# Optimization experiments

Hardware: AMD Instinct MI355X
Metric: run time of the kernel (lower is better)

## Reference

```python
import jax, jax.numpy as jnp
import numpy as np

RADIUS = 8
EPS = 1e-4


def box1d(x, r, axis):
    # sliding-window sum of width 2r+1 with border clamping (cumsum trick),
    # matching the classic guided-filter boxfilter (same as torch cumsum impl).
    n = x.shape[axis]
    c = jnp.cumsum(x, axis=axis)
    pad_shape = list(x.shape)
    pad_shape[axis] = 1
    s = jnp.concatenate([jnp.zeros(pad_shape, x.dtype), c], axis=axis)  # prefix sums, s[0]=0
    i = jnp.arange(n)
    hi = jnp.clip(i + r, 0, n - 1) + 1
    lo = jnp.clip(i - r - 1, -1, n - 1) + 1
    return jnp.take(s, hi, axis=axis) - jnp.take(s, lo, axis=axis)


def boxfilter2d(x, r):
    return box1d(box1d(x, r, -2), r, -1)


def setup_inputs() -> dict:
    key = jax.random.key(0)
    k1, k2 = jax.random.split(key)
    x = jax.random.uniform(k1, (4, 4, 1024, 1024), dtype=jnp.float32)
    guide = jax.random.uniform(k2, (4, 3, 1024, 1024), dtype=jnp.float32)
    return {"x": x, "guide": guide}


def guidedfilter2d_color(guide, src, r, eps):
    B, C, H, W = src.shape
    N = boxfilter2d(jnp.ones((B, 1, H, W), src.dtype), r)          # (B,1,H,W)
    mean_I = boxfilter2d(guide, r) / N                              # (B,3,H,W)
    mean_p = boxfilter2d(src, r) / N                                # (B,C,H,W)

    Ip = guide[:, :, None] * src[:, None]                           # (B,3,C,H,W)
    mean_Ip = boxfilter2d(Ip, r) / N[:, None]                       # (B,3,C,H,W)
    cov_Ip = mean_Ip - mean_I[:, :, None] * mean_p[:, None]         # (B,3,C,H,W)

    II = guide[:, :, None] * guide[:, None]                         # (B,3,3,H,W)
    var_I = boxfilter2d(II, r) / N[:, None] - mean_I[:, :, None] * mean_I[:, None]
    # eps added on the diagonal only, as in the torch code
    rr = var_I[:, 0, 0] + eps
    rg = var_I[:, 0, 1]
    rb = var_I[:, 0, 2]
    gg = var_I[:, 1, 1] + eps
    gb = var_I[:, 1, 2]
    bb = var_I[:, 2, 2] + eps

    det = (rr * gg * bb + 2.0 * rg * gb * rb
           - rb * gg * rb - rg * rg * bb - rr * gb * gb)            # (B,H,W)
    inv_rr = (gg * bb - gb * gb) / det
    inv_rg = -(rg * bb - rb * gb) / det
    inv_rb = (rg * gb - rb * gg) / det
    inv_gg = (rr * bb - rb * rb) / det
    inv_gb = -(rr * gb - rb * rg) / det
    inv_bb = (rr * gg - rg * rg) / det

    inv_sigma = jnp.stack([
        jnp.stack([inv_rr, inv_rg, inv_rb], 1),
        jnp.stack([inv_rg, inv_gg, inv_gb], 1),
        jnp.stack([inv_rb, inv_gb, inv_bb], 1),
    ], 1)                                                            # (B,3,3,H,W)

    a = jnp.einsum('bichw,bijhw->bjchw', cov_Ip, inv_sigma)          # (B,3,C,H,W)
    b = mean_p - jnp.einsum('bichw,bihw->bchw', a, mean_I)           # (B,C,H,W)

    mean_a = boxfilter2d(a, r) / N[:, None]                          # (B,3,C,H,W)
    mean_b = boxfilter2d(b, r) / N                                   # (B,C,H,W)

    q = jnp.einsum('bichw,bihw->bchw', mean_a, guide) + mean_b       # (B,C,H,W)
    return q


def reference(x, guide):
    return guidedfilter2d_color(guide, x, RADIUS, EPS)
```

## Files before the change

### kernel.cpp

```cpp
#include <hip/hip_runtime.h>

#define HH 1024
#define WW 1024
#define RAD 8
#define EPSF 1e-4f
#define HWSZ (HH * WW)
#define NPLB 16
#define T2 216
#define NTL 5
#define RROWS 4
#define V3R 32

__device__ __forceinline__ float4 f4add(float4 a, float4 b) {
  return make_float4(a.x + b.x, a.y + b.y, a.z + b.z, a.w + b.w);
}
__device__ __forceinline__ float4 f4sub(float4 a, float4 b) {
  return make_float4(a.x - b.x, a.y - b.y, a.z - b.z, a.w - b.w);
}
__device__ __forceinline__ float4 f4mul(float4 a, float4 b) {
  return make_float4(a.x * b.x, a.y * b.y, a.z * b.z, a.w * b.w);
}

__device__ __forceinline__ float wave_incl_scan(float v) {
  int t;
  t = __builtin_amdgcn_update_dpp(0, __float_as_int(v), 0x111, 0xf, 0xf, false);
  v += __int_as_float(t);
  t = __builtin_amdgcn_update_dpp(0, __float_as_int(v), 0x112, 0xf, 0xf, false);
  v += __int_as_float(t);
  t = __builtin_amdgcn_update_dpp(0, __float_as_int(v), 0x114, 0xf, 0xf, false);
  v += __int_as_float(t);
  t = __builtin_amdgcn_update_dpp(0, __float_as_int(v), 0x118, 0xf, 0xf, false);
  v += __int_as_float(t);
  t = __builtin_amdgcn_update_dpp(0, __float_as_int(v), 0x142, 0xa, 0xf, false);
  v += __int_as_float(t);
  t = __builtin_amdgcn_update_dpp(0, __float_as_int(v), 0x143, 0xc, 0xf, false);
  v += __int_as_float(t);
  return v;
}

__global__ __launch_bounds__(256, 2) void k_stats_solve(
    const float* __restrict__ x, const float* __restrict__ g,
    float* __restrict__ ws, int b0) {
  const int lane = threadIdx.x & 63;
  const int w = threadIdx.x >> 6;
  const int bi = blockIdx.y;
  const int gw = blockIdx.x * 4 + w;
  const int rowblk = gw / NTL;
  const int tix = gw - rowblk * NTL;
  const int y0 = rowblk * RROWS;
  const int b = b0 + bi;
  float* wsb = ws + (size_t)bi * NPLB * HWSZ;
  const int F = tix * T2;
  const int E = F - 20;
  const int relmax = (WW - 1) - E;
  const int col0 = E + 4 * lane;
  const bool ldok = (col0 >= 0) && (col0 < WW);

  const float* gp0 = g + (size_t)(b * 3 + 0) * HWSZ;
  const float* gp1 = g + (size_t)(b * 3 + 1) * HWSZ;
  const float* gp2 = g + (size_t)(b * 3 + 2) * HWSZ;
  const float* sp0 = x + (size_t)(b * 4 + 0) * HWSZ;
  const float* sp1 = x + (size_t)(b * 4 + 1) * HWSZ;
  const float* sp2 = x + (size_t)(b * 4 + 2) * HWSZ;
  const float* sp3 = x + (size_t)(b * 4 + 3) * HWSZ;

  const int cbase = E + 12 + 4 * lane;
  float nxinv[4];
#pragma unroll
  for (int j = 0; j < 4; ++j) {
    const int c = cbase + j;
    const int nx = min(c + RAD, WW - 1) - max(c - RAD, 0) + 1;
    nxinv[j] = 1.0f / (float)nx;
  }
  const bool abok = (lane <= 58) && (cbase >= 0) && (cbase < WW);
  const int qmax = relmax - 12;
  const int nstore = min(54, (WW - F) >> 2);
  const bool stok = lane < nstore;

  float4 s[25];
#pragma unroll
  for (int i = 0; i < 25; ++i) s[i] = make_float4(0.f, 0.f, 0.f, 0.f);

  const float4 Z4 = make_float4(0.f, 0.f, 0.f, 0.f);

  auto row_acc = [&](int yy, bool add) {
    if (yy < 0 || yy >= HH) return;
    const int off = yy * WW + col0;
    const float4 G0 = ldok ? *(const float4*)(gp0 + off) : Z4;
    const float4 G1 = ldok ? *(const float4*)(gp1 + off) : Z4;
    const float4 G2 = ldok ? *(const float4*)(gp2 + off) : Z4;
    const float4 S0 = ldok ? *(const float4*)(sp0 + off) : Z4;
    const float4 S1 = ldok ? *(const float4*)(sp1 + off) : Z4;
    const float4 S2 = ldok ? *(const float4*)(sp2 + off) : Z4;
    const float4 S3 = ldok ? *(const float4*)(sp3 + off) : Z4;
#define ACC(idx, val)                          \
  do {                                         \
    const float4 t_ = (val);                   \
    s[idx] = add ? f4add(s[idx], t_) : f4sub(s[idx], t_); \
  } while (0)
    ACC(0, G0); ACC(1, G1); ACC(2, G2);
    ACC(3, S0); ACC(4, S1); ACC(5, S2); ACC(6, S3);
    ACC(7, f4mul(G0, S0)); ACC(8, f4mul(G0, S1));
    ACC(9, f4mul(G0, S2)); ACC(10, f4mul(G0, S3));
    ACC(11, f4mul(G1, S0)); ACC(12, f4mul(G1, S1));
    ACC(13, f4mul(G1, S2)); ACC(14, f4mul(G1, S3));
    ACC(15, f4mul(G2, S0)); ACC(16, f4mul(G2, S1));
    ACC(17, f4mul(G2, S2)); ACC(18, f4mul(G2, S3));
    ACC(19, f4mul(G0, G0)); ACC(20, f4mul(G0, G1)); ACC(21, f4mul(G0, G2));
    ACC(22, f4mul(G1, G1)); ACC(23, f4mul(G1, G2)); ACC(24, f4mul(G2, G2));
#undef ACC
  };

  auto hbox4 = [&](float4 sv) -> float4 {
    const float s1 = sv.x + sv.y, s2 = s1 + sv.z, ts = s2 + sv.w;
    const float incl = wave_incl_scan(ts);
    const float base = incl - ts;
    const float P0 = base + sv.x, P1 = base + s1, P2 = base + s2, P3 = incl;
    const float PW = __shfl(P3, min(relmax >> 2, 63));
    const float h0 = __shfl(P0, lane + 5), h1 = __shfl(P1, lane + 5);
    const float h2 = __shfl(P2, lane + 5), h3 = __shfl(P3, lane + 5);
    const float l1 = __shfl(P0, lane + 1), l2 = __shfl(P1, lane + 1);
    const float l3 = __shfl(P2, lane + 1);
    const int r0 = 4 * lane + 12;
    float4 o;
    o.x = ((r0 + 8 <= relmax) ? h0 : PW) - ((E + r0 >= 9) ? P3 : 0.f);
    o.y = ((r0 + 9 <= relmax) ? h1 : PW) - ((E + r0 + 1 >= 9) ? l1 : 0.f);
    o.z = ((r0 + 10 <= relmax) ? h2 : PW) - ((E + r0 + 2 >= 9) ? l2 : 0.f);
    o.w = ((r0 + 11 <= relmax) ? h3 : PW) - ((E + r0 + 3 >= 9) ? l3 : 0.f);
    return o;
  };

  for (int yy = y0 - RAD; yy <= y0 + RAD; ++yy) row_acc(yy, true);

  for (int row = y0; row < y0 + RROWS; ++row) {
    const int ny = min(row + RAD, HH - 1) - max(row - RAD, 0) + 1;
    const float invny = 1.0f / (float)ny;
    float invN[4];
#pragma unroll
    for (int j = 0; j < 4; ++j) invN[j] = invny * nxinv[j];

    float mI[3][4];
#pragma unroll
    for (int k = 0; k < 3; ++k) {
      const float4 t = hbox4(s[k]);
      mI[k][0] = t.x * invN[0]; mI[k][1] = t.y * invN[1];
      mI[k][2] = t.z * invN[2]; mI[k][3] = t.w * invN[3];
    }
    float inv[6][4];
    {
      const float4 t19 = hbox4(s[19]), t20 = hbox4(s[20]), t21 = hbox4(s[21]);
      const float4 t22 = hbox4(s[22]), t23 = hbox4(s[23]), t24 = hbox4(s[24]);
      const float v19[4] = {t19.x, t19.y, t19.z, t19.w};
      const float v20[4] = {t20.x, t20.y, t20.z, t20.w};
      const float v21[4] = {t21.x, t21.y, t21.z, t21.w};
      const float v22[4] = {t22.x, t22.y, t22.z, t22.w};
      const float v23[4] = {t23.x, t23.y, t23.z, t23.w};
      const float v24[4] = {t24.x, t24.y, t24.z, t24.w};
#pragma unroll
      for (int j = 0; j < 4; ++j) {
        const float rr = v19[j] * invN[j] - mI[0][j] * mI[0][j] + EPSF;
        const float rg = v20[j] * invN[j] - mI[0][j] * mI[1][j];
        const float rb = v21[j] * invN[j] - mI[0][j] * mI[2][j];
        const float gg = v22[j] * invN[j] - mI[1][j] * mI[1][j] + EPSF;
        const float gb = v23[j] * invN[j] - mI[1][j] * mI[2][j];
        const float bb = v24[j] * invN[j] - mI[2][j] * mI[2][j] + EPSF;
        const float det = rr * gg * bb + 2.f * rg * gb * rb
                        - rb * gg * rb - rg * rg * bb - rr * gb * gb;
        const float idet = 1.0f / det;
        inv[0][j] = (gg * bb - gb * gb) * idet;
        inv[1][j] = (rb * gb - rg * bb) * idet;
        inv[2][j] = (rg * gb - rb * gg) * idet;
        inv[3][j] = (rr * bb - rb * rb) * idet;
        inv[4][j] = (rb * rg - rr * gb) * idet;
        inv[5][j] = (rr * gg - rg * rg) * idet;
      }
    }

    const size_t obase = (size_t)row * WW + F + 4 * lane;
    auto phaseB = [&](float4 vv, int plane) {
      const float s1 = vv.x + vv.y, s2 = s1 + vv.z, ts = s2 + vv.w;
      const float incl = wave_incl_scan(ts);
      const float base = incl - ts;
      const float Q0 = base + vv.x, Q1 = base + s1, Q2 = base + s2, Q3 = incl;
      const float PW2 = __shfl(Q3, min(qmax >> 2, 63));
      const float h0 = __shfl(Q0, lane + 4), h1 = __shfl(Q1, lane + 4);
      const float h2 = __shfl(Q2, lane + 4), h3 = __shfl(Q3, lane + 4);
      const float lm1 = __shfl(Q3, lane - 1);
      const int qf0 = 8 + 4 * lane;
      float4 o;
      o.x = ((qf0 + 8 <= qmax) ? h0 : PW2) - ((qf0 >= 9) ? lm1 : 0.f);
      o.y = ((qf0 + 9 <= qmax) ? h1 : PW2) - Q0;
      o.z = ((qf0 + 10 <= qmax) ? h2 : PW2) - Q1;
      o.w = ((qf0 + 11 <= qmax) ? h3 : PW2) - Q2;
      if (stok) *(float4*)(wsb + (size_t)plane * HWSZ + obase) = o;
    };

#pragma unroll
    for (int cc = 0; cc < 4; ++cc) {
      const float4 tmp = hbox4(s[3 + cc]);
      const float4 tq0 = hbox4(s[7 + cc]);
      const float4 tq1 = hbox4(s[11 + cc]);
      const float4 tq2 = hbox4(s[15 + cc]);
      const float mp[4] = {tmp.x, tmp.y, tmp.z, tmp.w};
      const float q0[4] = {tq0.x, tq0.y, tq0.z, tq0.w};
      const float q1[4] = {tq1.x, tq1.y, tq1.z, tq1.w};
      const float q2[4] = {tq2.x, tq2.y, tq2.z, tq2.w};
      float4 a0v, a1v, a2v, bv;
      float* pa0 = &a0v.x; float* pa1 = &a1v.x;
      float* pa2 = &a2v.x; float* pbv = &bv.x;
#pragma unroll
      for (int j = 0; j < 4; ++j) {
        const float m = mp[j] * invN[j];
        const float c0v = q0[j] * invN[j] - mI[0][j] * m;
        const float c1v = q1[j] * invN[j] - mI[1][j] * m;
        const float c2v = q2[j] * invN[j] - mI[2][j] * m;
        const float a0 = c0v * inv[0][j] + c1v * inv[1][j] + c2v * inv[2][j];
        const float a1 = c0v * inv[1][j] + c1v * inv[3][j] + c2v * inv[4][j];
        const float a2 = c0v * inv[2][j] + c1v * inv[4][j] + c2v * inv[5][j];
        const float b_ = m - (a0 * mI[0][j] + a1 * mI[1][j] + a2 * mI[2][j]);
        pa0[j] = abok ? a0 : 0.f;
        pa1[j] = abok ? a1 : 0.f;
        pa2[j] = abok ? a2 : 0.f;
        pbv[j] = abok ? b_ : 0.f;
      }
      phaseB(a0v, cc);
      phaseB(a1v, 4 + cc);
      phaseB(a2v, 8 + cc);
      phaseB(bv, 12 + cc);
    }

    row_acc(row + RAD + 1, true);
    row_acc(row - RAD, false);
  }
}

__global__ __launch_bounds__(256) void k_vbox_comb(const float* __restrict__ ws_,
                                                   const float* __restrict__ g,
                                                   float* __restrict__ out, int b0) {
  const int col = blockIdx.x * 256 + threadIdx.x;
  const int y0 = blockIdx.y * V3R;
  const int b = b0 + blockIdx.z;
  const float* wsb = ws_ + (size_t)blockIdx.z * NPLB * HWSZ;
  const float* gp0 = g + (size_t)(b * 3 + 0) * HWSZ;
  const float* gp1 = g + (size_t)(b * 3 + 1) * HWSZ;
  const float* gp2 = g + (size_t)(b * 3 + 2) * HWSZ;
  float* op0 = out + (size_t)(b * 4 + 0) * HWSZ;
  float* op1 = out + (size_t)(b * 4 + 1) * HWSZ;
  float* op2 = out + (size_t)(b * 4 + 2) * HWSZ;
  float* op3 = out + (size_t)(b * 4 + 3) * HWSZ;

  float acc[16];
#pragma unroll
  for (int i = 0; i < 16; ++i) acc[i] = 0.f;

  auto row_op = [&](int y, bool add) {
    const int off = y * WW + col;
#pragma unroll
    for (int i = 0; i < 16; ++i) {
      const float v = wsb[(size_t)i * HWSZ + off];
      acc[i] = add ? (acc[i] + v) : (acc[i] - v);
    }
  };

  for (int yy = y0 - RAD; yy <= y0 + RAD; ++yy)
    if (yy >= 0 && yy < HH) row_op(yy, true);

  const int nx = min(col + RAD, WW - 1) - max(col - RAD, 0) + 1;
  const float invnx = 1.0f / (float)nx;

  for (int y = y0; y < y0 + V3R; ++y) {
    const int ny = min(y + RAD, HH - 1) - max(y - RAD, 0) + 1;
    const float invN = invnx / (float)ny;
    const size_t off = (size_t)y * WW + col;
    const float g0 = gp0[off], g1 = gp1[off], g2 = gp2[off];
    op0[off] = (acc[0] * g0 + acc[4] * g1 + acc[8]  * g2 + acc[12]) * invN;
    op1[off] = (acc[1] * g0 + acc[5] * g1 + acc[9]  * g2 + acc[13]) * invN;
    op2[off] = (acc[2] * g0 + acc[6] * g1 + acc[10] * g2 + acc[14]) * invN;
    op3[off] = (acc[3] * g0 + acc[7] * g1 + acc[11] * g2 + acc[15]) * invN;
    const int ye = y + RAD + 1;
    if (ye < HH) row_op(ye, true);
    const int yl = y - RAD;
    if (yl >= 0) row_op(yl, false);
  }
}

extern "C" void kernel_launch(void* const* d_in, const int* in_sizes, int n_in,
                              void* d_out, int out_size, void* d_ws, size_t ws_size,
                              hipStream_t stream) {
  const float* x = (const float*)d_in[0];
  const float* g = (const float*)d_in[1];
  float* out = (float*)d_out;
  float* ws = (float*)d_ws;
  const size_t perBatchBytes = (size_t)NPLB * HWSZ * sizeof(float);
  int nb = (int)(ws_size / perBatchBytes);
  if (nb < 1) nb = 1;
  if (nb > 4) nb = 4;
  for (int b0 = 0; b0 < 4; b0 += nb) {
    const int nbc = (4 - b0 < nb) ? (4 - b0) : nb;
    dim3 gA((HH / RROWS) * NTL / 4, nbc);
    dim3 gB(WW / 256, HH / V3R, nbc);
    hipLaunchKernelGGL(k_stats_solve, gA, dim3(256), 0, stream, x, g, ws, b0);
    hipLaunchKernelGGL(k_vbox_comb, gB, dim3(256), 0, stream, ws, g, out, b0);
  }
}
```

Measured before the change: 514.6 us.

## Interleave scan/shuffle stages, raise stats occupancy, split vbox kernel per channel

The stats kernel's launch bound rises from 2 to 4 blocks per SM, and its horizontal box filters are split into prefix-scan, shuffle-tap and combine stages. Pairs of planes are software-pipelined so one plane's shuffles overlap the next plane's scan, and the per-column math is rewritten as float4 vector ops with lane predicates hoisted out of the row loop. The vertical-box kernel now launches one block per output channel, keeping 4 accumulators instead of 16, which gives four times more blocks and lower register pressure. The risk is spilling of the 25 float4 accumulators under the tighter register budget, and guide loads repeated across channels in the second kernel.

```diff
diff --git a/kernel.cpp b/kernel.cpp
--- a/kernel.cpp
+++ b/kernel.cpp
@@ -20,6 +20,12 @@
 __device__ __forceinline__ float4 f4mul(float4 a, float4 b) {
   return make_float4(a.x * b.x, a.y * b.y, a.z * b.z, a.w * b.w);
 }
+__device__ __forceinline__ float4 f4adds(float4 a, float c) {
+  return make_float4(a.x + c, a.y + c, a.z + c, a.w + c);
+}
+__device__ __forceinline__ float4 f4scale(float4 a, float c) {
+  return make_float4(a.x * c, a.y * c, a.z * c, a.w * c);
+}
 
 __device__ __forceinline__ float wave_incl_scan(float v) {
   int t;
@@ -38,7 +44,17 @@
   return v;
 }
 
-__global__ __launch_bounds__(256, 2) void k_stats_solve(
+struct TapsA { float h0, h1, h2, h3, l1, l2, l3, pw; };
+struct TapsB { float h0, h1, h2, h3, lm, pw; };
+
+__device__ __forceinline__ float4 pre4(float4 v) {
+  const float s1 = v.x + v.y, s2 = s1 + v.z, ts = s2 + v.w;
+  const float incl = wave_incl_scan(ts);
+  const float base = incl - ts;
+  return make_float4(base + v.x, base + s1, base + s2, incl);
+}
+
+__global__ __launch_bounds__(256, 4) void k_stats_solve(
     const float* __restrict__ x, const float* __restrict__ g,
     float* __restrict__ ws, int b0) {
   const int lane = threadIdx.x & 63;
@@ -65,22 +81,70 @@
   const float* sp3 = x + (size_t)(b * 4 + 3) * HWSZ;
 
   const int cbase = E + 12 + 4 * lane;
-  float nxinv[4];
+  float4 nxinvv;
+  {
+    float t[4];
 #pragma unroll
-  for (int j = 0; j < 4; ++j) {
-    const int c = cbase + j;
-    const int nx = min(c + RAD, WW - 1) - max(c - RAD, 0) + 1;
-    nxinv[j] = 1.0f / (float)nx;
+    for (int j = 0; j < 4; ++j) {
+      const int c = cbase + j;
+      const int nx = min(c + RAD, WW - 1) - max(c - RAD, 0) + 1;
+      t[j] = 1.0f / (float)nx;
+    }
+    nxinvv = make_float4(t[0], t[1], t[2], t[3]);
   }
   const bool abok = (lane <= 58) && (cbase >= 0) && (cbase < WW);
   const int qmax = relmax - 12;
   const int nstore = min(54, (WW - F) >> 2);
   const bool stok = lane < nstore;
+  const int pwlA = min(relmax >> 2, 63);
+  const int pwlB = min(qmax >> 2, 63);
+  const int r0 = 4 * lane + 12;
+  const int qf0 = 8 + 4 * lane;
+  const bool ha0 = (r0 + 8 <= relmax), ha1 = (r0 + 9 <= relmax),
+             ha2 = (r0 + 10 <= relmax), ha3 = (r0 + 11 <= relmax);
+  const bool la0 = (E + r0 >= 9), la1 = (E + r0 + 1 >= 9),
+             la2 = (E + r0 + 2 >= 9), la3 = (E + r0 + 3 >= 9);
+  const bool hb0 = (qf0 + 8 <= qmax), hb1 = (qf0 + 9 <= qmax),
+             hb2 = (qf0 + 10 <= qmax), hb3 = (qf0 + 11 <= qmax);
+  const bool lb0 = (qf0 >= 9);
+
+  auto tapsA = [&](float4 P) -> TapsA {
+    TapsA t;
+    t.h0 = __shfl(P.x, lane + 5); t.h1 = __shfl(P.y, lane + 5);
+    t.h2 = __shfl(P.z, lane + 5); t.h3 = __shfl(P.w, lane + 5);
+    t.l1 = __shfl(P.x, lane + 1); t.l2 = __shfl(P.y, lane + 1);
+    t.l3 = __shfl(P.z, lane + 1);
+    t.pw = __shfl(P.w, pwlA);
+    return t;
+  };
+  auto consA = [&](float4 P, TapsA t) -> float4 {
+    float4 o;
+    o.x = (ha0 ? t.h0 : t.pw) - (la0 ? P.w : 0.f);
+    o.y = (ha1 ? t.h1 : t.pw) - (la1 ? t.l1 : 0.f);
+    o.z = (ha2 ? t.h2 : t.pw) - (la2 ? t.l2 : 0.f);
+    o.w = (ha3 ? t.h3 : t.pw) - (la3 ? t.l3 : 0.f);
+    return o;
+  };
+  auto tapsB = [&](float4 Q) -> TapsB {
+    TapsB u;
+    u.h0 = __shfl(Q.x, lane + 4); u.h1 = __shfl(Q.y, lane + 4);
+    u.h2 = __shfl(Q.z, lane + 4); u.h3 = __shfl(Q.w, lane + 4);
+    u.lm = __shfl(Q.w, lane - 1);
+    u.pw = __shfl(Q.w, pwlB);
+    return u;
+  };
+  auto consB = [&](float4 Q, TapsB u) -> float4 {
+    float4 o;
+    o.x = (hb0 ? u.h0 : u.pw) - (lb0 ? u.lm : 0.f);
+    o.y = (hb1 ? u.h1 : u.pw) - Q.x;
+    o.z = (hb2 ? u.h2 : u.pw) - Q.y;
+    o.w = (hb3 ? u.h3 : u.pw) - Q.z;
+    return o;
+  };
 
   float4 s[25];
 #pragma unroll
   for (int i = 0; i < 25; ++i) s[i] = make_float4(0.f, 0.f, 0.f, 0.f);
-
   const float4 Z4 = make_float4(0.f, 0.f, 0.f, 0.f);
 
   auto row_acc = [&](int yy, bool add) {
@@ -93,10 +157,10 @@
     const float4 S1 = ldok ? *(const float4*)(sp1 + off) : Z4;
     const float4 S2 = ldok ? *(const float4*)(sp2 + off) : Z4;
     const float4 S3 = ldok ? *(const float4*)(sp3 + off) : Z4;
-#define ACC(idx, val)                          \
-  do {                                         \
-    const float4 t_ = (val);                   \
-    s[idx] = add ? f4add(s[idx], t_) : f4sub(s[idx], t_); \
+#define ACC(idx, val)                                       \
+  do {                                                      \
+    const float4 t_ = (val);                                \
+    s[idx] = add ? f4add(s[idx], t_) : f4sub(s[idx], t_);   \
   } while (0)
     ACC(0, G0); ACC(1, G1); ACC(2, G2);
     ACC(3, S0); ACC(4, S1); ACC(5, S2); ACC(6, S3);
@@ -111,123 +175,94 @@
 #undef ACC
   };
 
-  auto hbox4 = [&](float4 sv) -> float4 {
-    const float s1 = sv.x + sv.y, s2 = s1 + sv.z, ts = s2 + sv.w;
-    const float incl = wave_incl_scan(ts);
-    const float base = incl - ts;
-    const float P0 = base + sv.x, P1 = base + s1, P2 = base + s2, P3 = incl;
-    const float PW = __shfl(P3, min(relmax >> 2, 63));
-    const float h0 = __shfl(P0, lane + 5), h1 = __shfl(P1, lane + 5);
-    const float h2 = __shfl(P2, lane + 5), h3 = __shfl(P3, lane + 5);
-    const float l1 = __shfl(P0, lane + 1), l2 = __shfl(P1, lane + 1);
-    const float l3 = __shfl(P2, lane + 1);
-    const int r0 = 4 * lane + 12;
-    float4 o;
-    o.x = ((r0 + 8 <= relmax) ? h0 : PW) - ((E + r0 >= 9) ? P3 : 0.f);
-    o.y = ((r0 + 9 <= relmax) ? h1 : PW) - ((E + r0 + 1 >= 9) ? l1 : 0.f);
-    o.z = ((r0 + 10 <= relmax) ? h2 : PW) - ((E + r0 + 2 >= 9) ? l2 : 0.f);
-    o.w = ((r0 + 11 <= relmax) ? h3 : PW) - ((E + r0 + 3 >= 9) ? l3 : 0.f);
-    return o;
-  };
-
   for (int yy = y0 - RAD; yy <= y0 + RAD; ++yy) row_acc(yy, true);
 
   for (int row = y0; row < y0 + RROWS; ++row) {
     const int ny = min(row + RAD, HH - 1) - max(row - RAD, 0) + 1;
-    const float invny = 1.0f / (float)ny;
-    float invN[4];
-#pragma unroll
-    for (int j = 0; j < 4; ++j) invN[j] = invny * nxinv[j];
-
-    float mI[3][4];
-#pragma unroll
-    for (int k = 0; k < 3; ++k) {
-      const float4 t = hbox4(s[k]);
-      mI[k][0] = t.x * invN[0]; mI[k][1] = t.y * invN[1];
-      mI[k][2] = t.z * invN[2]; mI[k][3] = t.w * invN[3];
-    }
-    float inv[6][4];
-    {
-      const float4 t19 = hbox4(s[19]), t20 = hbox4(s[20]), t21 = hbox4(s[21]);
-      const float4 t22 = hbox4(s[22]), t23 = hbox4(s[23]), t24 = hbox4(s[24]);
-      const float v19[4] = {t19.x, t19.y, t19.z, t19.w};
-      const float v20[4] = {t20.x, t20.y, t20.z, t20.w};
-      const float v21[4] = {t21.x, t21.y, t21.z, t21.w};
-      const float v22[4] = {t22.x, t22.y, t22.z, t22.w};
-      const float v23[4] = {t23.x, t23.y, t23.z, t23.w};
-      const float v24[4] = {t24.x, t24.y, t24.z, t24.w};
-#pragma unroll
-      for (int j = 0; j < 4; ++j) {
-        const float rr = v19[j] * invN[j] - mI[0][j] * mI[0][j] + EPSF;
-        const float rg = v20[j] * invN[j] - mI[0][j] * mI[1][j];
-        const float rb = v21[j] * invN[j] - mI[0][j] * mI[2][j];
-        const float gg = v22[j] * invN[j] - mI[1][j] * mI[1][j] + EPSF;
-        const float gb = v23[j] * invN[j] - mI[1][j] * mI[2][j];
-        const float bb = v24[j] * invN[j] - mI[2][j] * mI[2][j] + EPSF;
-        const float det = rr * gg * bb + 2.f * rg * gb * rb
-                        - rb * gg * rb - rg * rg * bb - rr * gb * gb;
-        const float idet = 1.0f / det;
-        inv[0][j] = (gg * bb - gb * gb) * idet;
-        inv[1][j] = (rb * gb - rg * bb) * idet;
-        inv[2][j] = (rg * gb - rb * gg) * idet;
-        inv[3][j] = (rr * bb - rb * rb) * idet;
-        inv[4][j] = (rb * rg - rr * gb) * idet;
-        inv[5][j] = (rr * gg - rg * rg) * idet;
-      }
-    }
+    const float4 invNv = f4scale(nxinvv, 1.0f / (float)ny);
+
+    float4 Pa = pre4(s[0]); TapsA Ta = tapsA(Pa);
+    float4 Pb = pre4(s[1]);
+    const float4 c0 = consA(Pa, Ta); TapsA Tb = tapsA(Pb);
+    Pa = pre4(s[2]);
+    const float4 c1 = consA(Pb, Tb); Ta = tapsA(Pa);
+    Pb = pre4(s[19]);
+    const float4 c2 = consA(Pa, Ta); Tb = tapsA(Pb);
+    Pa = pre4(s[20]);
+    const float4 t19 = consA(Pb, Tb); Ta = tapsA(Pa);
+    Pb = pre4(s[21]);
+    const float4 t20 = consA(Pa, Ta); Tb = tapsA(Pb);
+    Pa = pre4(s[22]);
+    const float4 t21 = consA(Pb, Tb); Ta = tapsA(Pa);
+    Pb = pre4(s[23]);
+    const float4 t22 = consA(Pa, Ta); Tb = tapsA(Pb);
+    Pa = pre4(s[24]);
+    const float4 t23 = consA(Pb, Tb); Ta = tapsA(Pa);
+    const float4 t24 = consA(Pa, Ta);
+
+    const float4 mI0 = f4mul(c0, invNv);
+    const float4 mI1 = f4mul(c1, invNv);
+    const float4 mI2 = f4mul(c2, invNv);
+#define M(a, b) f4mul(a, b)
+    const float4 rr = f4adds(f4sub(M(t19, invNv), M(mI0, mI0)), EPSF);
+    const float4 rg = f4sub(M(t20, invNv), M(mI0, mI1));
+    const float4 rb = f4sub(M(t21, invNv), M(mI0, mI2));
+    const float4 gg = f4adds(f4sub(M(t22, invNv), M(mI1, mI1)), EPSF);
+    const float4 gb = f4sub(M(t23, invNv), M(mI1, mI2));
+    const float4 bb = f4adds(f4sub(M(t24, invNv), M(mI2, mI2)), EPSF);
+    const float4 det = f4sub(
+        f4sub(f4sub(f4add(M(M(rr, gg), bb), f4scale(M(M(rg, gb), rb), 2.f)),
+                    M(M(rb, gg), rb)),
+              M(M(rg, rg), bb)),
+        M(M(rr, gb), gb));
+    const float4 idet =
+        make_float4(1.f / det.x, 1.f / det.y, 1.f / det.z, 1.f / det.w);
+    const float4 iv0 = M(f4sub(M(gg, bb), M(gb, gb)), idet);
+    const float4 iv1 = M(f4sub(M(rb, gb), M(rg, bb)), idet);
+    const float4 iv2 = M(f4sub(M(rg, gb), M(rb, gg)), idet);
+    const float4 iv3 = M(f4sub(M(rr, bb), M(rb, rb)), idet);
+    const float4 iv4 = M(f4sub(M(rb, rg), M(rr, gb)), idet);
+    const float4 iv5 = M(f4sub(M(rr, gg), M(rg, rg)), idet);
 
     const size_t obase = (size_t)row * WW + F + 4 * lane;
-    auto phaseB = [&](float4 vv, int plane) {
-      const float s1 = vv.x + vv.y, s2 = s1 + vv.z, ts = s2 + vv.w;
-      const float incl = wave_incl_scan(ts);
-      const float base = incl - ts;
-      const float Q0 = base + vv.x, Q1 = base + s1, Q2 = base + s2, Q3 = incl;
-      const float PW2 = __shfl(Q3, min(qmax >> 2, 63));
-      const float h0 = __shfl(Q0, lane + 4), h1 = __shfl(Q1, lane + 4);
-      const float h2 = __shfl(Q2, lane + 4), h3 = __shfl(Q3, lane + 4);
-      const float lm1 = __shfl(Q3, lane - 1);
-      const int qf0 = 8 + 4 * lane;
-      float4 o;
-      o.x = ((qf0 + 8 <= qmax) ? h0 : PW2) - ((qf0 >= 9) ? lm1 : 0.f);
-      o.y = ((qf0 + 9 <= qmax) ? h1 : PW2) - Q0;
-      o.z = ((qf0 + 10 <= qmax) ? h2 : PW2) - Q1;
-      o.w = ((qf0 + 11 <= qmax) ? h3 : PW2) - Q2;
+    auto stB = [&](float4 o, int plane) {
       if (stok) *(float4*)(wsb + (size_t)plane * HWSZ + obase) = o;
     };
 
 #pragma unroll
     for (int cc = 0; cc < 4; ++cc) {
-      const float4 tmp = hbox4(s[3 + cc]);
-      const float4 tq0 = hbox4(s[7 + cc]);
-      const float4 tq1 = hbox4(s[11 + cc]);
-      const float4 tq2 = hbox4(s[15 + cc]);
-      const float mp[4] = {tmp.x, tmp.y, tmp.z, tmp.w};
-      const float q0[4] = {tq0.x, tq0.y, tq0.z, tq0.w};
-      const float q1[4] = {tq1.x, tq1.y, tq1.z, tq1.w};
-      const float q2[4] = {tq2.x, tq2.y, tq2.z, tq2.w};
-      float4 a0v, a1v, a2v, bv;
-      float* pa0 = &a0v.x; float* pa1 = &a1v.x;
-      float* pa2 = &a2v.x; float* pbv = &bv.x;
-#pragma unroll
-      for (int j = 0; j < 4; ++j) {
-        const float m = mp[j] * invN[j];
-        const float c0v = q0[j] * invN[j] - mI[0][j] * m;
-        const float c1v = q1[j] * invN[j] - mI[1][j] * m;
-        const float c2v = q2[j] * invN[j] - mI[2][j] * m;
-        const float a0 = c0v * inv[0][j] + c1v * inv[1][j] + c2v * inv[2][j];
-        const float a1 = c0v * inv[1][j] + c1v * inv[3][j] + c2v * inv[4][j];
-        const float a2 = c0v * inv[2][j] + c1v * inv[4][j] + c2v * inv[5][j];
-        const float b_ = m - (a0 * mI[0][j] + a1 * mI[1][j] + a2 * mI[2][j]);
-        pa0[j] = abok ? a0 : 0.f;
-        pa1[j] = abok ? a1 : 0.f;
-        pa2[j] = abok ? a2 : 0.f;
-        pbv[j] = abok ? b_ : 0.f;
-      }
-      phaseB(a0v, cc);
-      phaseB(a1v, 4 + cc);
-      phaseB(a2v, 8 + cc);
-      phaseB(bv, 12 + cc);
+      float4 Pc = pre4(s[3 + cc]); TapsA Tc = tapsA(Pc);
+      float4 Pd = pre4(s[7 + cc]);
+      const float4 tmp = consA(Pc, Tc); TapsA Td = tapsA(Pd);
+      Pc = pre4(s[11 + cc]);
+      const float4 tq0 = consA(Pd, Td); Tc = tapsA(Pc);
+      Pd = pre4(s[15 + cc]);
+      const float4 tq1 = consA(Pc, Tc); Td = tapsA(Pd);
+      const float4 tq2 = consA(Pd, Td);
+
+      const float4 m = M(tmp, invNv);
+      const float4 cv0 = f4sub(M(tq0, invNv), M(mI0, m));
+      const float4 cv1 = f4sub(M(tq1, invNv), M(mI1, m));
+      const float4 cv2 = f4sub(M(tq2, invNv), M(mI2, m));
+      float4 a0 = f4add(f4add(M(cv0, iv0), M(cv1, iv1)), M(cv2, iv2));
+      float4 a1 = f4add(f4add(M(cv0, iv1), M(cv1, iv3)), M(cv2, iv4));
+      float4 a2 = f4add(f4add(M(cv0, iv2), M(cv1, iv4)), M(cv2, iv5));
+      float4 bv = f4sub(m, f4add(f4add(M(a0, mI0), M(a1, mI1)), M(a2, mI2)));
+      a0 = abok ? a0 : Z4;
+      a1 = abok ? a1 : Z4;
+      a2 = abok ? a2 : Z4;
+      bv = abok ? bv : Z4;
+
+      float4 Qa = pre4(a0); TapsB Ua = tapsB(Qa);
+      float4 Qb = pre4(a1);
+      stB(consB(Qa, Ua), cc); TapsB Ub = tapsB(Qb);
+      Qa = pre4(a2);
+      stB(consB(Qb, Ub), 4 + cc); Ua = tapsB(Qa);
+      Qb = pre4(bv);
+      stB(consB(Qa, Ua), 8 + cc); Ub = tapsB(Qb);
+      stB(consB(Qb, Ub), 12 + cc);
     }
+#undef M
 
     row_acc(row + RAD + 1, true);
     row_acc(row - RAD, false);
@@ -239,27 +274,25 @@
                                                    float* __restrict__ out, int b0) {
   const int col = blockIdx.x * 256 + threadIdx.x;
   const int y0 = blockIdx.y * V3R;
-  const int b = b0 + blockIdx.z;
-  const float* wsb = ws_ + (size_t)blockIdx.z * NPLB * HWSZ;
+  const int zz = blockIdx.z;
+  const int bi = zz >> 2;
+  const int cc = zz & 3;
+  const int b = b0 + bi;
+  const float* A0 = ws_ + (size_t)bi * NPLB * HWSZ + (size_t)cc * HWSZ;
+  const float* A1 = A0 + (size_t)4 * HWSZ;
+  const float* A2 = A0 + (size_t)8 * HWSZ;
+  const float* Bp = A0 + (size_t)12 * HWSZ;
   const float* gp0 = g + (size_t)(b * 3 + 0) * HWSZ;
   const float* gp1 = g + (size_t)(b * 3 + 1) * HWSZ;
   const float* gp2 = g + (size_t)(b * 3 + 2) * HWSZ;
-  float* op0 = out + (size_t)(b * 4 + 0) * HWSZ;
-  float* op1 = out + (size_t)(b * 4 + 1) * HWSZ;
-  float* op2 = out + (size_t)(b * 4 + 2) * HWSZ;
-  float* op3 = out + (size_t)(b * 4 + 3) * HWSZ;
-
-  float acc[16];
-#pragma unroll
-  for (int i = 0; i < 16; ++i) acc[i] = 0.f;
-
+  float* op = out + (size_t)(b * 4 + cc) * HWSZ;
+
+  float a0 = 0.f, a1 = 0.f, a2 = 0.f, ab = 0.f;
   auto row_op = [&](int y, bool add) {
     const int off = y * WW + col;
-#pragma unroll
-    for (int i = 0; i < 16; ++i) {
-      const float v = wsb[(size_t)i * HWSZ + off];
-      acc[i] = add ? (acc[i] + v) : (acc[i] - v);
-    }
+    const float v0 = A0[off], v1 = A1[off], v2 = A2[off], v3 = Bp[off];
+    if (add) { a0 += v0; a1 += v1; a2 += v2; ab += v3; }
+    else     { a0 -= v0; a1 -= v1; a2 -= v2; ab -= v3; }
   };
 
   for (int yy = y0 - RAD; yy <= y0 + RAD; ++yy)
@@ -273,10 +306,7 @@
     const float invN = invnx / (float)ny;
     const size_t off = (size_t)y * WW + col;
     const float g0 = gp0[off], g1 = gp1[off], g2 = gp2[off];
-    op0[off] = (acc[0] * g0 + acc[4] * g1 + acc[8]  * g2 + acc[12]) * invN;
-    op1[off] = (acc[1] * g0 + acc[5] * g1 + acc[9]  * g2 + acc[13]) * invN;
-    op2[off] = (acc[2] * g0 + acc[6] * g1 + acc[10] * g2 + acc[14]) * invN;
-    op3[off] = (acc[3] * g0 + acc[7] * g1 + acc[11] * g2 + acc[15]) * invN;
+    op[off] = (a0 * g0 + a1 * g1 + a2 * g2 + ab) * invN;
     const int ye = y + RAD + 1;
     if (ye < HH) row_op(ye, true);
     const int yl = y - RAD;
@@ -298,7 +328,7 @@
   for (int b0 = 0; b0 < 4; b0 += nb) {
     const int nbc = (4 - b0 < nb) ? (4 - b0) : nb;
     dim3 gA((HH / RROWS) * NTL / 4, nbc);
-    dim3 gB(WW / 256, HH / V3R, nbc);
+    dim3 gB(WW / 256, HH / V3R, nbc * 4);
     hipLaunchKernelGGL(k_stats_solve, gA, dim3(256), 0, stream, x, g, ws, b0);
     hipLaunchKernelGGL(k_vbox_comb, gB, dim3(256), 0, stream, ws, g, out, b0);
   }
```

Result: slower. 1.536 ms (+198.5%).
